# Kernel optimization log

Measured on AMD Instinct MI355X. Metric: run time of the kernel, lower is better.

Reference implementation:

```python
import jax, jax.numpy as jnp
import numpy as np

WEIGHT_SP = 0.1
BANDWIDTH = 0.5
EPS = 1e-5


def _l2_normalize(v, axis, eps=1e-12):
    # matches torch F.normalize(p=2): x / max(||x||, eps)
    n = jnp.sqrt(jnp.sum(v * v, axis=axis, keepdims=True))
    return v / jnp.maximum(n, eps)


def _compute_meshgrid(N, H, W):
    rows = jnp.arange(H, dtype=jnp.float32) / (H + 1)
    cols = jnp.arange(W, dtype=jnp.float32) / (W + 1)
    gr, gc = jnp.meshgrid(rows, cols, indexing="ij")
    grid = jnp.stack([gr, gc])[None]  # (1, 2, H, W)
    return jnp.broadcast_to(grid, (N, 2, H, W))


def _l2_distance(x, y):
    # Faithful to the torch code; its broadcasting is only valid for N == 1.
    N, C, H, W = x.shape
    xv = x.reshape(N, C, -1)
    yv = y.reshape(N, C, -1)
    x_s = jnp.sum(xv ** 2, axis=1)          # (N, HW)
    y_s = jnp.sum(yv ** 2, axis=1)          # (N, HW)
    A = jnp.einsum("nci,ncj->nij", yv, xv)  # (N, HW, HW)
    dist = y_s - 2.0 * A + x_s.T            # same broadcast as torch (N==1)
    dist = jnp.swapaxes(dist, 1, 2)         # transpose(1,2); reshape is no-op
    return jnp.maximum(dist, 0.0)


def _cosine_distance(x, y):
    y_mu = jnp.mean(y, axis=(0, 2, 3), keepdims=True)   # (1, C, 1, 1)
    xn = _l2_normalize(x - y_mu, axis=1)
    yn = _l2_normalize(y - y_mu, axis=1)
    N, C = x.shape[:2]
    xn = xn.reshape(N, C, -1)
    yn = yn.reshape(N, C, -1)
    cos = jnp.einsum("nci,ncj->nij", xn, yn)            # (N, HW, HW)
    return 1.0 - cos


def _relative_distance(dist, eps=1e-5):
    dmin = jnp.min(dist, axis=2, keepdims=True)
    return dist / (dmin + eps)


def _compute_cx(dist_tilde, bandwidth):
    w = jnp.exp((1.0 - dist_tilde) / bandwidth)
    return w / jnp.sum(w, axis=2, keepdims=True)


def setup_inputs() -> dict:
    key = jax.random.key(0)
    k1, k2 = jax.random.split(key)
    x = jax.random.normal(k1, (1, 512, 80, 80), dtype=jnp.float32)
    y = jax.random.normal(k2, (1, 512, 80, 80), dtype=jnp.float32)
    return {"x": x, "y": y}


def reference(x, y):
    N, C, H, W = x.shape
    # spatial branch
    grid = _compute_meshgrid(N, H, W)
    cx_sp = _compute_cx(_relative_distance(_l2_distance(grid, grid), 1e-5), BANDWIDTH)
    # feature branch (loss_type == 'cosine')
    cx_feat = _compute_cx(_relative_distance(_cosine_distance(x, y), EPS), BANDWIDTH)
    cx_combine = (1.0 - WEIGHT_SP) * cx_feat + WEIGHT_SP * cx_sp
    k_max = jnp.max(cx_combine, axis=2, keepdims=True)  # (N, HW, 1)
    cx = jnp.mean(k_max, axis=1)                        # (N, 1)
    return jnp.mean(-jnp.log(cx + EPS))
```

## Files before the change

### kernel.cpp

```cpp
#include <hip/hip_runtime.h>
#include <hip/hip_bf16.h>
#include <math.h>

#define HW 6400
#define NC 512
#define NH 80
#define NW 80
#define NCH 25
#define NSLOT 50
#define NCYS 8
#define JCH 256
#define TI 128
#define BK 64
#define NT16 400

typedef __attribute__((ext_vector_type(8))) short short8;
typedef __attribute__((ext_vector_type(4))) float v4f;

#define MU_OFF    0
#define INVD_OFF  512
#define GMAXP_OFF (512 + HW)
#define ZP_OFF    (GMAXP_OFF + HW*NSLOT)
#define WDP_OFF   (ZP_OFF + HW*NSLOT)
#define ACC_OFF   (WDP_OFF + HW*NCYS)
#define F32_FLOATS (ACC_OFF + 64)
#define XB_BYTE   ((size_t)(((F32_FLOATS*4) + 255) & ~255))
#define YB_BYTE   (XB_BYTE + (size_t)HW*NC*2)
#define G_BYTE    (YB_BYTE + (size_t)HW*NC*2)
#define G_BYTES   ((size_t)NT16 * NT16 * 256 * 2)

typedef __attribute__((address_space(1))) unsigned int uint_g;
typedef __attribute__((address_space(3))) unsigned int uint_l;
__device__ __forceinline__ void gload16(const void* g, void* l) {
    __builtin_amdgcn_global_load_lds((const uint_g*)g, (uint_l*)l, 16, 0, 0);
}

__global__ void k_mu(const float* __restrict__ y, float* __restrict__ mu) {
    int c = blockIdx.x;
    const float* yc = y + (size_t)c * HW;
    float s = 0.f;
    for (int i = threadIdx.x; i < HW; i += 256) s += yc[i];
    __shared__ float red[256];
    red[threadIdx.x] = s;
    __syncthreads();
    for (int off = 128; off > 0; off >>= 1) {
        if (threadIdx.x < off) red[threadIdx.x] += red[threadIdx.x + off];
        __syncthreads();
    }
    if (threadIdx.x == 0) mu[c] = red[0] * (1.0f / HW);
}

__global__ void k_sumsq(const float* __restrict__ x, const float* __restrict__ y,
                        const float* __restrict__ mu,
                        float* __restrict__ psx, float* __restrict__ psy) {
    int i = blockIdx.x * 256 + threadIdx.x;
    int c0 = blockIdx.y * 64;
    float sx = 0.f, sy = 0.f;
    for (int c = c0; c < c0 + 64; ++c) {
        float m = mu[c];
        float dx = x[(size_t)c * HW + i] - m;
        float dy = y[(size_t)c * HW + i] - m;
        sx = fmaf(dx, dx, sx);
        sy = fmaf(dy, dy, sy);
    }
    psx[(size_t)blockIdx.y * HW + i] = sx;
    psy[(size_t)blockIdx.y * HW + i] = sy;
}

__global__ void k_transpose(const float* __restrict__ x, const float* __restrict__ y,
                            const float* __restrict__ mu,
                            const float* __restrict__ psx, const float* __restrict__ psy,
                            unsigned short* __restrict__ xb, unsigned short* __restrict__ yb) {
    __shared__ float tile[64 * 68];
    __shared__ float ssinv[64];
    const int t = threadIdx.x;
    const int i0 = blockIdx.x * 64;
    const int c0 = blockIdx.y * 64;
    const int z = blockIdx.z;
    const float* src = z ? y : x;
    const float* ps  = z ? psy : psx;
    unsigned short* dst = z ? yb : xb;

    if (t < 64) {
        float s = 0.f;
        #pragma unroll
        for (int p = 0; p < 8; ++p) s += ps[(size_t)p * HW + i0 + t];
        ssinv[t] = 1.0f / fmaxf(sqrtf(s), 1e-12f);
    }
    __syncthreads();
    #pragma unroll 4
    for (int it = 0; it < 16; ++it) {
        int cl = it * 4 + (t >> 6);
        int il = t & 63;
        float v = (src[(size_t)(c0 + cl) * HW + i0 + il] - mu[c0 + cl]) * ssinv[il];
        tile[il * 68 + cl] = v;
    }
    __syncthreads();
    #pragma unroll
    for (int it = 0; it < 2; ++it) {
        int il = t >> 2;
        int seg = (t & 3) + it * 4;
        unsigned int pk[4];
        #pragma unroll
        for (int p = 0; p < 4; ++p) {
            float v0 = tile[il * 68 + seg * 8 + p * 2];
            float v1 = tile[il * 68 + seg * 8 + p * 2 + 1];
            __hip_bfloat16 h0 = __float2bfloat16(v0);
            __hip_bfloat16 h1 = __float2bfloat16(v1);
            unsigned short u0 = *reinterpret_cast<unsigned short*>(&h0);
            unsigned short u1 = *reinterpret_cast<unsigned short*>(&h1);
            pk[p] = (unsigned int)u0 | ((unsigned int)u1 << 16);
        }
        uint4 val = make_uint4(pk[0], pk[1], pk[2], pk[3]);
        *(uint4*)&dst[(size_t)(i0 + il) * NC + c0 + seg * 8] = val;
    }
}

template <typename F>
__device__ __forceinline__ void gemm_driver(const unsigned short* __restrict__ Xb,
                                            const unsigned short* __restrict__ Yb,
                                            F&& consume) {
    __shared__ char sA[TI * BK * 2];
    __shared__ char sB[TI * BK * 2];
    const int t = threadIdx.x;
    const int w = t >> 6, l = t & 63;
    const int wr = w >> 1, wc = w & 1;
    const int lr = l & 15, lg = l >> 4;
    const int i0 = blockIdx.x * TI;
    const int jbase = blockIdx.y * JCH;

    int aoff[4][2], boff[4][2];
    #pragma unroll
    for (int mt = 0; mt < 4; ++mt) {
        int row = wr * 64 + mt * 16 + lr;
        #pragma unroll
        for (int ks = 0; ks < 2; ++ks) {
            int seg = ks * 4 + lg;
            aoff[mt][ks] = row * 128 + ((seg ^ (row & 7)) * 16);
        }
    }
    #pragma unroll
    for (int nt = 0; nt < 4; ++nt) {
        int row = wc * 64 + nt * 16 + lr;
        #pragma unroll
        for (int ks = 0; ks < 2; ++ks) {
            int seg = ks * 4 + lg;
            boff[nt][ks] = row * 128 + ((seg ^ (row & 7)) * 16);
        }
    }

    const int strow = l >> 3;
    const int stcol = ((l & 7) ^ strow) * 8;
    char* dA0 = sA + (w * 4 + 0) * 1024;
    char* dA1 = sA + (w * 4 + 1) * 1024;
    char* dA2 = sA + (w * 4 + 2) * 1024;
    char* dA3 = sA + (w * 4 + 3) * 1024;
    char* dB0 = sB + (w * 4 + 0) * 1024;
    char* dB1 = sB + (w * 4 + 1) * 1024;
    char* dB2 = sB + (w * 4 + 2) * 1024;
    char* dB3 = sB + (w * 4 + 3) * 1024;
    const unsigned short* ga = Xb + (size_t)(i0 + w * 32 + strow) * NC + stcol;
    const unsigned short* gb0 = Yb + (size_t)(jbase + w * 32 + strow) * NC + stcol;

    #pragma unroll 1
    for (int jt = 0; jt < JCH; jt += TI) {
        const unsigned short* gb = gb0 + (size_t)jt * NC;
        v4f acc[4][4];
        #pragma unroll
        for (int mt = 0; mt < 4; ++mt)
            #pragma unroll
            for (int nt = 0; nt < 4; ++nt)
                acc[mt][nt] = (v4f){0.f, 0.f, 0.f, 0.f};

        #pragma unroll 1
        for (int kt = 0; kt < NC; kt += BK) {
            __syncthreads();
            gload16(ga + kt,           dA0);
            gload16(ga + 8  * NC + kt, dA1);
            gload16(ga + 16 * NC + kt, dA2);
            gload16(ga + 24 * NC + kt, dA3);
            gload16(gb + kt,           dB0);
            gload16(gb + 8  * NC + kt, dB1);
            gload16(gb + 16 * NC + kt, dB2);
            gload16(gb + 24 * NC + kt, dB3);
            __syncthreads();
            #pragma unroll
            for (int ks = 0; ks < 2; ++ks) {
                short8 af[4], bf[4];
                #pragma unroll
                for (int mt = 0; mt < 4; ++mt) af[mt] = *(const short8*)&sA[aoff[mt][ks]];
                #pragma unroll
                for (int nt = 0; nt < 4; ++nt) bf[nt] = *(const short8*)&sB[boff[nt][ks]];
                #pragma unroll
                for (int mt = 0; mt < 4; ++mt)
                    #pragma unroll
                    for (int nt = 0; nt < 4; ++nt)
                        acc[mt][nt] = __builtin_amdgcn_mfma_f32_16x16x32_bf16(
                            af[mt], bf[nt], acc[mt][nt], 0, 0, 0);
            }
        }
        consume(acc, jt);
    }
}

__device__ __forceinline__ void rmax_epilogue(float (&rmax)[16], float* gmaxp,
                                              int i0, int wr, int wc, int lr, int lg) {
    #pragma unroll
    for (int u = 0; u < 16; ++u) {
        float v = rmax[u];
        v = fmaxf(v, __shfl_xor(v, 1));
        v = fmaxf(v, __shfl_xor(v, 2));
        v = fmaxf(v, __shfl_xor(v, 4));
        v = fmaxf(v, __shfl_xor(v, 8));
        if (lr == 0) {
            int row = i0 + wr * 64 + (u >> 2) * 16 + lg * 4 + (u & 3);
            gmaxp[(size_t)row * NSLOT + blockIdx.y * 2 + wc] = v;
        }
    }
}

__global__ __launch_bounds__(256, 2) void k_pass1s(const unsigned short* __restrict__ Xb,
                                                   const unsigned short* __restrict__ Yb,
                                                   float* __restrict__ gmaxp,
                                                   unsigned int* __restrict__ G2) {
    const int t = threadIdx.x;
    const int w = t >> 6, l = t & 63;
    const int wr = w >> 1, wc = w & 1;
    const int lr = l & 15, lg = l >> 4;
    const int i0 = blockIdx.x * TI;
    const int jbase = blockIdx.y * JCH;
    float rmax[16];
    #pragma unroll
    for (int u = 0; u < 16; ++u) rmax[u] = -3.0e38f;

    gemm_driver(Xb, Yb, [&](v4f (&acc)[4][4], int jt) {
        #pragma unroll
        for (int mt = 0; mt < 4; ++mt) {
            size_t rbase = (size_t)(i0 / 16 + wr * 4 + mt) * (NT16 * 128);
            #pragma unroll
            for (int nt = 0; nt < 4; ++nt) {
                int ct = (jbase + jt) / 16 + wc * 4 + nt;
                unsigned int pk0, pk1;
                {
                    __hip_bfloat16 h0 = __float2bfloat16(acc[mt][nt][0]);
                    __hip_bfloat16 h1 = __float2bfloat16(acc[mt][nt][1]);
                    __hip_bfloat16 h2 = __float2bfloat16(acc[mt][nt][2]);
                    __hip_bfloat16 h3 = __float2bfloat16(acc[mt][nt][3]);
                    pk0 = (unsigned int)*(unsigned short*)&h0 | ((unsigned int)*(unsigned short*)&h1 << 16);
                    pk1 = (unsigned int)*(unsigned short*)&h2 | ((unsigned int)*(unsigned short*)&h3 << 16);
                }
                *(uint2*)&G2[(rbase + (size_t)ct * 128 + l * 2)] = make_uint2(pk0, pk1);
                #pragma unroll
                for (int r = 0; r < 4; ++r)
                    rmax[mt * 4 + r] = fmaxf(rmax[mt * 4 + r], acc[mt][nt][r]);
            }
        }
    });
    rmax_epilogue(rmax, gmaxp, i0, wr, wc, lr, lg);
}

__global__ __launch_bounds__(256) void k_pass2s(const unsigned int* __restrict__ G2,
                                                const float* __restrict__ gmaxp,
                                                float* __restrict__ zp,
                                                float* __restrict__ wdp) {
    const int t = threadIdx.x;
    const int w = t >> 6, l = t & 63;
    const int lr = l & 15, lg = l >> 4;
    const int rt = blockIdx.x * 4 + w;
    const int cy = blockIdx.y;

    float m = -3.0e38f;
    {
        int row = rt * 16 + lr;
        #pragma unroll
        for (int k = 0; k < 13; ++k) {
            int s = lg + 4 * k;
            if (s < NSLOT) m = fmaxf(m, gmaxp[(size_t)row * NSLOT + s]);
        }
        m = fmaxf(m, __shfl_xor(m, 16));
        m = fmaxf(m, __shfl_xor(m, 32));
    }
    float inv_lr = 1.0f / ((1.0f - m) + 1e-5f);
    float c1[4], c2[4];
    #pragma unroll
    for (int r = 0; r < 4; ++r) {
        float iv = __shfl(inv_lr, lg * 4 + r);
        c2[r] = 2.0f * iv;
        c1[r] = 2.0f - 2.0f * iv;
    }

    const uint2* base = (const uint2*)G2 + (size_t)rt * (NT16 * 64) + l;
    float zs[4] = {0.f, 0.f, 0.f, 0.f};
    #pragma unroll 4
    for (int ct = cy * 50; ct < cy * 50 + 50; ++ct) {
        uint2 v = base[(size_t)ct * 64];
        float g0 = __uint_as_float((v.x & 0xFFFFu) << 16);
        float g1 = __uint_as_float(v.x & 0xFFFF0000u);
        float g2 = __uint_as_float((v.y & 0xFFFFu) << 16);
        float g3 = __uint_as_float(v.y & 0xFFFF0000u);
        zs[0] += __expf(fmaf(c2[0], g0, c1[0]));
        zs[1] += __expf(fmaf(c2[1], g1, c1[1]));
        zs[2] += __expf(fmaf(c2[2], g2, c1[2]));
        zs[3] += __expf(fmaf(c2[3], g3, c1[3]));
    }
    float wd[4] = {0.f, 0.f, 0.f, 0.f};
    if (rt / 50 == cy) {
        uint2 v = base[(size_t)rt * 64];
        float g[4];
        g[0] = __uint_as_float((v.x & 0xFFFFu) << 16);
        g[1] = __uint_as_float(v.x & 0xFFFF0000u);
        g[2] = __uint_as_float((v.y & 0xFFFFu) << 16);
        g[3] = __uint_as_float(v.y & 0xFFFF0000u);
        #pragma unroll
        for (int r = 0; r < 4; ++r)
            if (lr == lg * 4 + r) wd[r] = __expf(fmaf(c2[r], g[r], c1[r]));
    }
    #pragma unroll
    for (int r = 0; r < 4; ++r) {
        float z = zs[r], d = wd[r];
        z += __shfl_xor(z, 1);  d += __shfl_xor(d, 1);
        z += __shfl_xor(z, 2);  d += __shfl_xor(d, 2);
        z += __shfl_xor(z, 4);  d += __shfl_xor(d, 4);
        z += __shfl_xor(z, 8);  d += __shfl_xor(d, 8);
        if (lr == 0) {
            int row = rt * 16 + lg * 4 + r;
            zp[(size_t)row * NCYS + cy] = z;
            wdp[(size_t)row * NCYS + cy] = d;
        }
    }
}

__global__ void k_kmax_s(const float* __restrict__ zp, const float* __restrict__ wdp,
                         const float* __restrict__ gmaxp, float* __restrict__ accum,
                         int* __restrict__ counter, float* __restrict__ out) {
    int i = blockIdx.x * 256 + threadIdx.x;
    float Z = 0.f, wd = 0.f, gmax = -3.0e38f;
    #pragma unroll
    for (int s = 0; s < NCYS; ++s) {
        Z += zp[(size_t)i * NCYS + s];
        wd += wdp[(size_t)i * NCYS + s];
    }
    #pragma unroll
    for (int s = 0; s < NSLOT; ++s) gmax = fmaxf(gmax, gmaxp[(size_t)i * NSLOT + s]);
    float dmin = 1.0f - gmax;
    float inv = 1.0f / (dmin + 1e-5f);
    float wmx = __expf(2.0f - 2.0f * dmin * inv);
    float invZ = 1.0f / Z;
    float kmax = fmaxf(0.9f * wmx * invZ, 0.9f * wd * invZ + 0.1f);

    __shared__ float red[256];
    red[threadIdx.x] = kmax;
    __syncthreads();
    for (int off = 128; off > 0; off >>= 1) {
        if (threadIdx.x < off) red[threadIdx.x] += red[threadIdx.x + off];
        __syncthreads();
    }
    if (threadIdx.x == 0) {
        atomicAdd(accum, red[0]);
        __threadfence();
        int n = atomicAdd(counter, 1);
        if (n == (int)gridDim.x - 1) {
            float total = atomicAdd(accum, 0.0f);
            out[0] = -logf(total * (1.0f / HW) + 1e-5f);
        }
    }
}

__global__ __launch_bounds__(256, 2) void k_pass1(const unsigned short* __restrict__ Xb,
                                                  const unsigned short* __restrict__ Yb,
                                                  float* __restrict__ gmaxp) {
    const int t = threadIdx.x;
    const int w = t >> 6, l = t & 63;
    const int wr = w >> 1, wc = w & 1;
    const int lr = l & 15, lg = l >> 4;
    const int i0 = blockIdx.x * TI;
    float rmax[16];
    #pragma unroll
    for (int u = 0; u < 16; ++u) rmax[u] = -3.0e38f;
    gemm_driver(Xb, Yb, [&](v4f (&acc)[4][4], int jt) {
        (void)jt;
        #pragma unroll
        for (int mt = 0; mt < 4; ++mt)
            #pragma unroll
            for (int r = 0; r < 4; ++r) {
                float mm = acc[mt][0][r];
                #pragma unroll
                for (int nt = 1; nt < 4; ++nt) mm = fmaxf(mm, acc[mt][nt][r]);
                rmax[mt * 4 + r] = fmaxf(rmax[mt * 4 + r], mm);
            }
    });
    rmax_epilogue(rmax, gmaxp, i0, wr, wc, lr, lg);
}

__global__ void k_invd(const float* __restrict__ gmaxp, float* __restrict__ invd) {
    int i = blockIdx.x * 256 + threadIdx.x;
    float m = -3.0e38f;
    #pragma unroll
    for (int s = 0; s < NSLOT; ++s) m = fmaxf(m, gmaxp[(size_t)i * NSLOT + s]);
    invd[i] = 1.0f / ((1.0f - m) + 1e-5f);
}

__global__ __launch_bounds__(256, 2) void k_pass2(const unsigned short* __restrict__ Xb,
                                                  const unsigned short* __restrict__ Yb,
                                                  const float* __restrict__ invd,
                                                  float* __restrict__ zp) {
    const int t = threadIdx.x;
    const int w = t >> 6, l = t & 63;
    const int wr = w >> 1, wc = w & 1;
    const int lr = l & 15, lg = l >> 4;
    const int i0 = blockIdx.x * TI;
    float zs[16], c1[16], c2[16];
    #pragma unroll
    for (int u = 0; u < 16; ++u) {
        int row = i0 + wr * 64 + (u >> 2) * 16 + lg * 4 + (u & 3);
        float inv = invd[row];
        c2[u] = 2.0f * inv;
        c1[u] = 2.0f - 2.0f * inv;
        zs[u] = 0.f;
    }
    gemm_driver(Xb, Yb, [&](v4f (&acc)[4][4], int jt) {
        (void)jt;
        #pragma unroll
        for (int mt = 0; mt < 4; ++mt)
            #pragma unroll
            for (int r = 0; r < 4; ++r) {
                int u = mt * 4 + r;
                float s = 0.f;
                #pragma unroll
                for (int nt = 0; nt < 4; ++nt)
                    s += __expf(fmaf(c2[u], acc[mt][nt][r], c1[u]));
                zs[u] += s;
            }
    });
    #pragma unroll
    for (int u = 0; u < 16; ++u) {
        float z = zs[u];
        z += __shfl_xor(z, 1);
        z += __shfl_xor(z, 2);
        z += __shfl_xor(z, 4);
        z += __shfl_xor(z, 8);
        if (lr == 0) {
            int row = i0 + wr * 64 + (u >> 2) * 16 + lg * 4 + (u & 3);
            zp[(size_t)row * NSLOT + blockIdx.y * 2 + wc] = z;
        }
    }
}

__global__ void k_kmax(const float* __restrict__ zp, const float* __restrict__ gmaxp,
                       const unsigned short* __restrict__ Xb, const unsigned short* __restrict__ Yb,
                       float* __restrict__ accum, int* __restrict__ counter,
                       float* __restrict__ out) {
    int i = blockIdx.x * 256 + threadIdx.x;
    float Z = 0.f, gmax = -3.0e38f;
    #pragma unroll
    for (int s = 0; s < NSLOT; ++s) {
        Z += zp[(size_t)i * NSLOT + s];
        gmax = fmaxf(gmax, gmaxp[(size_t)i * NSLOT + s]);
    }
    float gii = 0.f;
    const uint2* xr = (const uint2*)(Xb + (size_t)i * NC);
    const uint2* yr = (const uint2*)(Yb + (size_t)i * NC);
    for (int c4 = 0; c4 < NC / 4; ++c4) {
        uint2 xa = xr[c4], ya = yr[c4];
        float x0 = __uint_as_float((xa.x & 0xFFFFu) << 16), y0 = __uint_as_float((ya.x & 0xFFFFu) << 16);
        float x1 = __uint_as_float(xa.x & 0xFFFF0000u),     y1 = __uint_as_float(ya.x & 0xFFFF0000u);
        float x2 = __uint_as_float((xa.y & 0xFFFFu) << 16), y2 = __uint_as_float((ya.y & 0xFFFFu) << 16);
        float x3 = __uint_as_float(xa.y & 0xFFFF0000u),     y3 = __uint_as_float(ya.y & 0xFFFF0000u);
        gii = fmaf(x0, y0, gii); gii = fmaf(x1, y1, gii);
        gii = fmaf(x2, y2, gii); gii = fmaf(x3, y3, gii);
    }
    float dmin = 1.0f - gmax;
    float inv = 1.0f / (dmin + 1e-5f);
    float wmx = __expf(2.0f - 2.0f * dmin * inv);
    float wii = __expf(2.0f - 2.0f * (1.0f - gii) * inv);
    float invZ = 1.0f / Z;
    float kmax = fmaxf(0.9f * wmx * invZ, 0.9f * wii * invZ + 0.1f);

    __shared__ float red[256];
    red[threadIdx.x] = kmax;
    __syncthreads();
    for (int off = 128; off > 0; off >>= 1) {
        if (threadIdx.x < off) red[threadIdx.x] += red[threadIdx.x + off];
        __syncthreads();
    }
    if (threadIdx.x == 0) {
        atomicAdd(accum, red[0]);
        __threadfence();
        int n = atomicAdd(counter, 1);
        if (n == (int)gridDim.x - 1) {
            float total = atomicAdd(accum, 0.0f);
            out[0] = -logf(total * (1.0f / HW) + 1e-5f);
        }
    }
}

extern "C" void kernel_launch(void* const* d_in, const int* in_sizes, int n_in,
                              void* d_out, int out_size, void* d_ws, size_t ws_size,
                              hipStream_t stream) {
    const float* x = (const float*)d_in[0];
    const float* y = (const float*)d_in[1];
    float* out = (float*)d_out;
    float* ws = (float*)d_ws;

    float* mu    = ws + MU_OFF;
    float* invd  = ws + INVD_OFF;
    float* gmaxp = ws + GMAXP_OFF;
    float* psx   = ws + GMAXP_OFF;
    float* psy   = ws + GMAXP_OFF + 8 * HW;
    float* zp    = ws + ZP_OFF;
    float* wdp   = ws + WDP_OFF;
    float* accum = ws + ACC_OFF;
    int*   counter = (int*)(accum + 1);
    unsigned short* Xb = (unsigned short*)((char*)d_ws + XB_BYTE);
    unsigned short* Yb = (unsigned short*)((char*)d_ws + YB_BYTE);
    unsigned int*   G2 = (unsigned int*)((char*)d_ws + G_BYTE);

    const bool bigws = ws_size >= (G_BYTE + G_BYTES);

    hipMemsetAsync(accum, 0, 8, stream);

    hipLaunchKernelGGL(k_mu, dim3(NC), dim3(256), 0, stream, y, mu);
    hipLaunchKernelGGL(k_sumsq, dim3(HW / 256, NC / 64), dim3(256), 0, stream, x, y, mu, psx, psy);
    hipLaunchKernelGGL(k_transpose, dim3(HW / 64, NC / 64, 2), dim3(256), 0, stream,
                       x, y, mu, psx, psy, Xb, Yb);

    dim3 grid(HW / TI, NCH);
    if (bigws) {
        hipLaunchKernelGGL(k_pass1s, grid, dim3(256), 0, stream, Xb, Yb, gmaxp, G2);
        hipLaunchKernelGGL(k_pass2s, dim3(NT16 / 4, NCYS), dim3(256), 0, stream, G2, gmaxp, zp, wdp);
        hipLaunchKernelGGL(k_kmax_s, dim3(HW / 256), dim3(256), 0, stream, zp, wdp, gmaxp,
                           accum, counter, out);
    } else {
        hipLaunchKernelGGL(k_pass1, grid, dim3(256), 0, stream, Xb, Yb, gmaxp);
        hipLaunchKernelGGL(k_invd, dim3(HW / 256), dim3(256), 0, stream, gmaxp, invd);
        hipLaunchKernelGGL(k_pass2, grid, dim3(256), 0, stream, Xb, Yb, invd, zp);
        hipLaunchKernelGGL(k_kmax, dim3(HW / 256), dim3(256), 0, stream, zp, gmaxp, Xb, Yb,
                           accum, counter, out);
    }
}
```

Baseline: 166.2 us.

## Fuse sum-of-squares into transpose and apply normalization in GEMM epilogue

Removes the separate sum-of-squares kernel: the transpose kernel now accumulates per-pixel squared norms via atomics from its shared tile, and a small kernel converts them to inverse norms. The bf16 operands are stored unnormalized, and the inverse norms are applied to the GEMM outputs in the epilogues. The big-workspace pass1 is rewritten as a standalone kernel with a 128x256 tile that computes the full K loop in one accumulator set, with no inner column loop. This trades one full read of x and y and a launch for atomics, a larger register and LDS footprint, and a different rounding point for the normalization.

```diff
diff --git a/kernel.cpp b/kernel.cpp
--- a/kernel.cpp
+++ b/kernel.cpp
@@ -18,12 +18,14 @@
 typedef __attribute__((ext_vector_type(4))) float v4f;
 
 #define MU_OFF    0
-#define INVD_OFF  512
-#define GMAXP_OFF (512 + HW)
-#define ZP_OFF    (GMAXP_OFF + HW*NSLOT)
+#define SQX_OFF   512
+#define SQY_OFF   (512 + HW)
+#define ACC_OFF   (512 + 2*HW)
+#define GMAXP_OFF (ACC_OFF + 64)
+#define INVD_OFF  (GMAXP_OFF + HW*NSLOT)
+#define ZP_OFF    (INVD_OFF + HW)
 #define WDP_OFF   (ZP_OFF + HW*NSLOT)
-#define ACC_OFF   (WDP_OFF + HW*NCYS)
-#define F32_FLOATS (ACC_OFF + 64)
+#define F32_FLOATS (WDP_OFF + HW*NCYS)
 #define XB_BYTE   ((size_t)(((F32_FLOATS*4) + 255) & ~255))
 #define YB_BYTE   (XB_BYTE + (size_t)HW*NC*2)
 #define G_BYTE    (YB_BYTE + (size_t)HW*NC*2)
@@ -50,52 +52,37 @@
     if (threadIdx.x == 0) mu[c] = red[0] * (1.0f / HW);
 }
 
-__global__ void k_sumsq(const float* __restrict__ x, const float* __restrict__ y,
-                        const float* __restrict__ mu,
-                        float* __restrict__ psx, float* __restrict__ psy) {
-    int i = blockIdx.x * 256 + threadIdx.x;
-    int c0 = blockIdx.y * 64;
-    float sx = 0.f, sy = 0.f;
-    for (int c = c0; c < c0 + 64; ++c) {
-        float m = mu[c];
-        float dx = x[(size_t)c * HW + i] - m;
-        float dy = y[(size_t)c * HW + i] - m;
-        sx = fmaf(dx, dx, sx);
-        sy = fmaf(dy, dy, sy);
-    }
-    psx[(size_t)blockIdx.y * HW + i] = sx;
-    psy[(size_t)blockIdx.y * HW + i] = sy;
-}
-
 __global__ void k_transpose(const float* __restrict__ x, const float* __restrict__ y,
                             const float* __restrict__ mu,
-                            const float* __restrict__ psx, const float* __restrict__ psy,
+                            float* __restrict__ sqx, float* __restrict__ sqy,
                             unsigned short* __restrict__ xb, unsigned short* __restrict__ yb) {
     __shared__ float tile[64 * 68];
-    __shared__ float ssinv[64];
     const int t = threadIdx.x;
     const int i0 = blockIdx.x * 64;
     const int c0 = blockIdx.y * 64;
     const int z = blockIdx.z;
     const float* src = z ? y : x;
-    const float* ps  = z ? psy : psx;
+    float* sq = z ? sqy : sqx;
     unsigned short* dst = z ? yb : xb;
 
-    if (t < 64) {
-        float s = 0.f;
-        #pragma unroll
-        for (int p = 0; p < 8; ++p) s += ps[(size_t)p * HW + i0 + t];
-        ssinv[t] = 1.0f / fmaxf(sqrtf(s), 1e-12f);
-    }
-    __syncthreads();
     #pragma unroll 4
     for (int it = 0; it < 16; ++it) {
         int cl = it * 4 + (t >> 6);
         int il = t & 63;
-        float v = (src[(size_t)(c0 + cl) * HW + i0 + il] - mu[c0 + cl]) * ssinv[il];
+        float v = src[(size_t)(c0 + cl) * HW + i0 + il] - mu[c0 + cl];
         tile[il * 68 + cl] = v;
     }
     __syncthreads();
+    {
+        int il = t & 63, q = t >> 6;
+        float s = 0.f;
+        #pragma unroll
+        for (int cl = q * 16; cl < q * 16 + 16; ++cl) {
+            float v = tile[il * 68 + cl];
+            s = fmaf(v, v, s);
+        }
+        atomicAdd(&sq[i0 + il], s);
+    }
     #pragma unroll
     for (int it = 0; it < 2; ++it) {
         int il = t >> 2;
@@ -113,6 +100,252 @@
         }
         uint4 val = make_uint4(pk[0], pk[1], pk[2], pk[3]);
         *(uint4*)&dst[(size_t)(i0 + il) * NC + c0 + seg * 8] = val;
+    }
+}
+
+__global__ void k_normfin(float* __restrict__ sqx, float* __restrict__ sqy) {
+    int i = blockIdx.x * 256 + threadIdx.x;
+    sqx[i] = 1.0f / fmaxf(sqrtf(sqx[i]), 1e-12f);
+    sqy[i] = 1.0f / fmaxf(sqrtf(sqy[i]), 1e-12f);
+}
+
+__device__ __forceinline__ void rmax_epilogue(float (&rmax)[16], float* gmaxp,
+                                              int i0, int wr, int wc, int lr, int lg) {
+    #pragma unroll
+    for (int u = 0; u < 16; ++u) {
+        float v = rmax[u];
+        v = fmaxf(v, __shfl_xor(v, 1));
+        v = fmaxf(v, __shfl_xor(v, 2));
+        v = fmaxf(v, __shfl_xor(v, 4));
+        v = fmaxf(v, __shfl_xor(v, 8));
+        if (lr == 0) {
+            int row = i0 + wr * 64 + (u >> 2) * 16 + lg * 4 + (u & 3);
+            gmaxp[(size_t)row * NSLOT + blockIdx.y * 2 + wc] = v;
+        }
+    }
+}
+
+__global__ __launch_bounds__(256, 2) void k_pass1s(const unsigned short* __restrict__ Xb,
+                                                   const unsigned short* __restrict__ Yb,
+                                                   const float* __restrict__ sxi,
+                                                   const float* __restrict__ syi,
+                                                   float* __restrict__ gmaxp,
+                                                   unsigned int* __restrict__ G2) {
+    __shared__ char sA[128 * 128];
+    __shared__ char sB[256 * 128];
+    const int t = threadIdx.x;
+    const int w = t >> 6, l = t & 63;
+    const int wr = w >> 1, wc = w & 1;
+    const int lr = l & 15, lg = l >> 4;
+    const int i0 = blockIdx.x * TI;
+    const int jbase = blockIdx.y * JCH;
+
+    int aoff[4][2], boff[8][2];
+    #pragma unroll
+    for (int mt = 0; mt < 4; ++mt) {
+        int row = wr * 64 + mt * 16 + lr;
+        #pragma unroll
+        for (int ks = 0; ks < 2; ++ks) {
+            int seg = ks * 4 + lg;
+            aoff[mt][ks] = row * 128 + ((seg ^ (row & 7)) * 16);
+        }
+    }
+    #pragma unroll
+    for (int nt = 0; nt < 8; ++nt) {
+        int row = wc * 128 + nt * 16 + lr;
+        #pragma unroll
+        for (int ks = 0; ks < 2; ++ks) {
+            int seg = ks * 4 + lg;
+            boff[nt][ks] = row * 128 + ((seg ^ (row & 7)) * 16);
+        }
+    }
+
+    const int strow = l >> 3;
+    const int stcol = ((l & 7) ^ strow) * 8;
+    const unsigned short* ga = Xb + (size_t)(i0 + w * 32 + strow) * NC + stcol;
+    const unsigned short* gb = Yb + (size_t)(jbase + w * 64 + strow) * NC + stcol;
+    char* dA = sA + w * 4096;
+    char* dB = sB + w * 8192;
+
+    v4f acc[4][8];
+    #pragma unroll
+    for (int mt = 0; mt < 4; ++mt)
+        #pragma unroll
+        for (int nt = 0; nt < 8; ++nt)
+            acc[mt][nt] = (v4f){0.f, 0.f, 0.f, 0.f};
+
+    #pragma unroll 1
+    for (int kt = 0; kt < NC; kt += BK) {
+        __syncthreads();
+        gload16(ga + kt,           dA);
+        gload16(ga + 8  * NC + kt, dA + 1024);
+        gload16(ga + 16 * NC + kt, dA + 2048);
+        gload16(ga + 24 * NC + kt, dA + 3072);
+        #pragma unroll
+        for (int it = 0; it < 8; ++it)
+            gload16(gb + it * 8 * NC + kt, dB + it * 1024);
+        __syncthreads();
+        #pragma unroll
+        for (int ks = 0; ks < 2; ++ks) {
+            short8 af[4], bf[8];
+            #pragma unroll
+            for (int mt = 0; mt < 4; ++mt) af[mt] = *(const short8*)&sA[aoff[mt][ks]];
+            #pragma unroll
+            for (int nt = 0; nt < 8; ++nt) bf[nt] = *(const short8*)&sB[boff[nt][ks]];
+            #pragma unroll
+            for (int mt = 0; mt < 4; ++mt)
+                #pragma unroll
+                for (int nt = 0; nt < 8; ++nt)
+                    acc[mt][nt] = __builtin_amdgcn_mfma_f32_16x16x32_bf16(
+                        af[mt], bf[nt], acc[mt][nt], 0, 0, 0);
+        }
+    }
+
+    float rsx[16];
+    #pragma unroll
+    for (int u = 0; u < 16; ++u) {
+        int row = i0 + wr * 64 + (u >> 2) * 16 + lg * 4 + (u & 3);
+        rsx[u] = sxi[row];
+    }
+    float rsy[8];
+    #pragma unroll
+    for (int nt = 0; nt < 8; ++nt)
+        rsy[nt] = syi[jbase + wc * 128 + nt * 16 + lr];
+
+    float rmax[16];
+    #pragma unroll
+    for (int u = 0; u < 16; ++u) rmax[u] = -3.0e38f;
+
+    #pragma unroll
+    for (int mt = 0; mt < 4; ++mt) {
+        size_t rbase = (size_t)(i0 / 16 + wr * 4 + mt) * (NT16 * 128);
+        #pragma unroll
+        for (int nt = 0; nt < 8; ++nt) {
+            int ct = jbase / 16 + wc * 8 + nt;
+            float g0 = acc[mt][nt][0] * rsx[mt * 4 + 0] * rsy[nt];
+            float g1 = acc[mt][nt][1] * rsx[mt * 4 + 1] * rsy[nt];
+            float g2 = acc[mt][nt][2] * rsx[mt * 4 + 2] * rsy[nt];
+            float g3 = acc[mt][nt][3] * rsx[mt * 4 + 3] * rsy[nt];
+            rmax[mt * 4 + 0] = fmaxf(rmax[mt * 4 + 0], g0);
+            rmax[mt * 4 + 1] = fmaxf(rmax[mt * 4 + 1], g1);
+            rmax[mt * 4 + 2] = fmaxf(rmax[mt * 4 + 2], g2);
+            rmax[mt * 4 + 3] = fmaxf(rmax[mt * 4 + 3], g3);
+            __hip_bfloat16 h0 = __float2bfloat16(g0);
+            __hip_bfloat16 h1 = __float2bfloat16(g1);
+            __hip_bfloat16 h2 = __float2bfloat16(g2);
+            __hip_bfloat16 h3 = __float2bfloat16(g3);
+            unsigned int pk0 = (unsigned int)*(unsigned short*)&h0 | ((unsigned int)*(unsigned short*)&h1 << 16);
+            unsigned int pk1 = (unsigned int)*(unsigned short*)&h2 | ((unsigned int)*(unsigned short*)&h3 << 16);
+            *(uint2*)&G2[rbase + (size_t)ct * 128 + l * 2] = make_uint2(pk0, pk1);
+        }
+    }
+    rmax_epilogue(rmax, gmaxp, i0, wr, wc, lr, lg);
+}
+
+__global__ __launch_bounds__(256) void k_pass2s(const unsigned int* __restrict__ G2,
+                                                const float* __restrict__ gmaxp,
+                                                float* __restrict__ zp,
+                                                float* __restrict__ wdp) {
+    const int t = threadIdx.x;
+    const int w = t >> 6, l = t & 63;
+    const int lr = l & 15, lg = l >> 4;
+    const int rt = blockIdx.x * 4 + w;
+    const int cy = blockIdx.y;
+
+    float m = -3.0e38f;
+    {
+        int row = rt * 16 + lr;
+        #pragma unroll
+        for (int k = 0; k < 13; ++k) {
+            int s = lg + 4 * k;
+            if (s < NSLOT) m = fmaxf(m, gmaxp[(size_t)row * NSLOT + s]);
+        }
+        m = fmaxf(m, __shfl_xor(m, 16));
+        m = fmaxf(m, __shfl_xor(m, 32));
+    }
+    float inv_lr = 1.0f / ((1.0f - m) + 1e-5f);
+    float c1[4], c2[4];
+    #pragma unroll
+    for (int r = 0; r < 4; ++r) {
+        float iv = __shfl(inv_lr, lg * 4 + r);
+        c2[r] = 2.0f * iv;
+        c1[r] = 2.0f - 2.0f * iv;
+    }
+
+    const uint2* base = (const uint2*)G2 + (size_t)rt * (NT16 * 64) + l;
+    float zs[4] = {0.f, 0.f, 0.f, 0.f};
+    #pragma unroll 4
+    for (int ct = cy * 50; ct < cy * 50 + 50; ++ct) {
+        uint2 v = base[(size_t)ct * 64];
+        float g0 = __uint_as_float((v.x & 0xFFFFu) << 16);
+        float g1 = __uint_as_float(v.x & 0xFFFF0000u);
+        float g2 = __uint_as_float((v.y & 0xFFFFu) << 16);
+        float g3 = __uint_as_float(v.y & 0xFFFF0000u);
+        zs[0] += __expf(fmaf(c2[0], g0, c1[0]));
+        zs[1] += __expf(fmaf(c2[1], g1, c1[1]));
+        zs[2] += __expf(fmaf(c2[2], g2, c1[2]));
+        zs[3] += __expf(fmaf(c2[3], g3, c1[3]));
+    }
+    float wd[4] = {0.f, 0.f, 0.f, 0.f};
+    if (rt / 50 == cy) {
+        uint2 v = base[(size_t)rt * 64];
+        float g[4];
+        g[0] = __uint_as_float((v.x & 0xFFFFu) << 16);
+        g[1] = __uint_as_float(v.x & 0xFFFF0000u);
+        g[2] = __uint_as_float((v.y & 0xFFFFu) << 16);
+        g[3] = __uint_as_float(v.y & 0xFFFF0000u);
+        #pragma unroll
+        for (int r = 0; r < 4; ++r)
+            if (lr == lg * 4 + r) wd[r] = __expf(fmaf(c2[r], g[r], c1[r]));
+    }
+    #pragma unroll
+    for (int r = 0; r < 4; ++r) {
+        float z = zs[r], d = wd[r];
+        z += __shfl_xor(z, 1);  d += __shfl_xor(d, 1);
+        z += __shfl_xor(z, 2);  d += __shfl_xor(d, 2);
+        z += __shfl_xor(z, 4);  d += __shfl_xor(d, 4);
+        z += __shfl_xor(z, 8);  d += __shfl_xor(d, 8);
+        if (lr == 0) {
+            int row = rt * 16 + lg * 4 + r;
+            zp[(size_t)row * NCYS + cy] = z;
+            wdp[(size_t)row * NCYS + cy] = d;
+        }
+    }
+}
+
+__global__ void k_kmax_s(const float* __restrict__ zp, const float* __restrict__ wdp,
+                         const float* __restrict__ gmaxp, float* __restrict__ accum,
+                         int* __restrict__ counter, float* __restrict__ out) {
+    int i = blockIdx.x * 256 + threadIdx.x;
+    float Z = 0.f, wd = 0.f, gmax = -3.0e38f;
+    #pragma unroll
+    for (int s = 0; s < NCYS; ++s) {
+        Z += zp[(size_t)i * NCYS + s];
+        wd += wdp[(size_t)i * NCYS + s];
+    }
+    #pragma unroll
+    for (int s = 0; s < NSLOT; ++s) gmax = fmaxf(gmax, gmaxp[(size_t)i * NSLOT + s]);
+    float dmin = 1.0f - gmax;
+    float inv = 1.0f / (dmin + 1e-5f);
+    float wmx = __expf(2.0f - 2.0f * dmin * inv);
+    float invZ = 1.0f / Z;
+    float kmax = fmaxf(0.9f * wmx * invZ, 0.9f * wd * invZ + 0.1f);
+
+    __shared__ float red[256];
+    red[threadIdx.x] = kmax;
+    __syncthreads();
+    for (int off = 128; off > 0; off >>= 1) {
+        if (threadIdx.x < off) red[threadIdx.x] += red[threadIdx.x + off];
+        __syncthreads();
+    }
+    if (threadIdx.x == 0) {
+        atomicAdd(accum, red[0]);
+        __threadfence();
+        int n = atomicAdd(counter, 1);
+        if (n == (int)gridDim.x - 1) {
+            float total = atomicAdd(accum, 0.0f);
+            out[0] = -logf(total * (1.0f / HW) + 1e-5f);
+        }
     }
 }
 
@@ -148,7 +381,6 @@
             boff[nt][ks] = row * 128 + ((seg ^ (row & 7)) * 16);
         }
     }
-
     const int strow = l >> 3;
     const int stcol = ((l & 7) ^ strow) * 8;
     char* dA0 = sA + (w * 4 + 0) * 1024;
@@ -203,191 +435,35 @@
     }
 }
 
-__device__ __forceinline__ void rmax_epilogue(float (&rmax)[16], float* gmaxp,
-                                              int i0, int wr, int wc, int lr, int lg) {
-    #pragma unroll
-    for (int u = 0; u < 16; ++u) {
-        float v = rmax[u];
-        v = fmaxf(v, __shfl_xor(v, 1));
-        v = fmaxf(v, __shfl_xor(v, 2));
-        v = fmaxf(v, __shfl_xor(v, 4));
-        v = fmaxf(v, __shfl_xor(v, 8));
-        if (lr == 0) {
-            int row = i0 + wr * 64 + (u >> 2) * 16 + lg * 4 + (u & 3);
-            gmaxp[(size_t)row * NSLOT + blockIdx.y * 2 + wc] = v;
-        }
-    }
-}
-
-__global__ __launch_bounds__(256, 2) void k_pass1s(const unsigned short* __restrict__ Xb,
-                                                   const unsigned short* __restrict__ Yb,
-                                                   float* __restrict__ gmaxp,
-                                                   unsigned int* __restrict__ G2) {
+__global__ __launch_bounds__(256, 2) void k_pass1(const unsigned short* __restrict__ Xb,
+                                                  const unsigned short* __restrict__ Yb,
+                                                  const float* __restrict__ sxi,
+                                                  const float* __restrict__ syi,
+                                                  float* __restrict__ gmaxp) {
     const int t = threadIdx.x;
     const int w = t >> 6, l = t & 63;
     const int wr = w >> 1, wc = w & 1;
     const int lr = l & 15, lg = l >> 4;
     const int i0 = blockIdx.x * TI;
     const int jbase = blockIdx.y * JCH;
-    float rmax[16];
-    #pragma unroll
-    for (int u = 0; u < 16; ++u) rmax[u] = -3.0e38f;
-
+    float rsx[16], rmax[16];
+    #pragma unroll
+    for (int u = 0; u < 16; ++u) {
+        int row = i0 + wr * 64 + (u >> 2) * 16 + lg * 4 + (u & 3);
+        rsx[u] = sxi[row];
+        rmax[u] = -3.0e38f;
+    }
     gemm_driver(Xb, Yb, [&](v4f (&acc)[4][4], int jt) {
         #pragma unroll
-        for (int mt = 0; mt < 4; ++mt) {
-            size_t rbase = (size_t)(i0 / 16 + wr * 4 + mt) * (NT16 * 128);
+        for (int nt = 0; nt < 4; ++nt) {
+            float sy = syi[jbase + jt + (wc * 4 + nt) * 16 + lr];
             #pragma unroll
-            for (int nt = 0; nt < 4; ++nt) {
-                int ct = (jbase + jt) / 16 + wc * 4 + nt;
-                unsigned int pk0, pk1;
-                {
-                    __hip_bfloat16 h0 = __float2bfloat16(acc[mt][nt][0]);
-                    __hip_bfloat16 h1 = __float2bfloat16(acc[mt][nt][1]);
-                    __hip_bfloat16 h2 = __float2bfloat16(acc[mt][nt][2]);
-                    __hip_bfloat16 h3 = __float2bfloat16(acc[mt][nt][3]);
-                    pk0 = (unsigned int)*(unsigned short*)&h0 | ((unsigned int)*(unsigned short*)&h1 << 16);
-                    pk1 = (unsigned int)*(unsigned short*)&h2 | ((unsigned int)*(unsigned short*)&h3 << 16);
-                }
-                *(uint2*)&G2[(rbase + (size_t)ct * 128 + l * 2)] = make_uint2(pk0, pk1);
+            for (int mt = 0; mt < 4; ++mt)
                 #pragma unroll
                 for (int r = 0; r < 4; ++r)
-                    rmax[mt * 4 + r] = fmaxf(rmax[mt * 4 + r], acc[mt][nt][r]);
-            }
-        }
-    });
-    rmax_epilogue(rmax, gmaxp, i0, wr, wc, lr, lg);
-}
-
-__global__ __launch_bounds__(256) void k_pass2s(const unsigned int* __restrict__ G2,
-                                                const float* __restrict__ gmaxp,
-                                                float* __restrict__ zp,
-                                                float* __restrict__ wdp) {
-    const int t = threadIdx.x;
-    const int w = t >> 6, l = t & 63;
-    const int lr = l & 15, lg = l >> 4;
-    const int rt = blockIdx.x * 4 + w;
-    const int cy = blockIdx.y;
-
-    float m = -3.0e38f;
-    {
-        int row = rt * 16 + lr;
-        #pragma unroll
-        for (int k = 0; k < 13; ++k) {
-            int s = lg + 4 * k;
-            if (s < NSLOT) m = fmaxf(m, gmaxp[(size_t)row * NSLOT + s]);
-        }
-        m = fmaxf(m, __shfl_xor(m, 16));
-        m = fmaxf(m, __shfl_xor(m, 32));
-    }
-    float inv_lr = 1.0f / ((1.0f - m) + 1e-5f);
-    float c1[4], c2[4];
-    #pragma unroll
-    for (int r = 0; r < 4; ++r) {
-        float iv = __shfl(inv_lr, lg * 4 + r);
-        c2[r] = 2.0f * iv;
-        c1[r] = 2.0f - 2.0f * iv;
-    }
-
-    const uint2* base = (const uint2*)G2 + (size_t)rt * (NT16 * 64) + l;
-    float zs[4] = {0.f, 0.f, 0.f, 0.f};
-    #pragma unroll 4
-    for (int ct = cy * 50; ct < cy * 50 + 50; ++ct) {
-        uint2 v = base[(size_t)ct * 64];
-        float g0 = __uint_as_float((v.x & 0xFFFFu) << 16);
-        float g1 = __uint_as_float(v.x & 0xFFFF0000u);
-        float g2 = __uint_as_float((v.y & 0xFFFFu) << 16);
-        float g3 = __uint_as_float(v.y & 0xFFFF0000u);
-        zs[0] += __expf(fmaf(c2[0], g0, c1[0]));
-        zs[1] += __expf(fmaf(c2[1], g1, c1[1]));
-        zs[2] += __expf(fmaf(c2[2], g2, c1[2]));
-        zs[3] += __expf(fmaf(c2[3], g3, c1[3]));
-    }
-    float wd[4] = {0.f, 0.f, 0.f, 0.f};
-    if (rt / 50 == cy) {
-        uint2 v = base[(size_t)rt * 64];
-        float g[4];
-        g[0] = __uint_as_float((v.x & 0xFFFFu) << 16);
-        g[1] = __uint_as_float(v.x & 0xFFFF0000u);
-        g[2] = __uint_as_float((v.y & 0xFFFFu) << 16);
-        g[3] = __uint_as_float(v.y & 0xFFFF0000u);
-        #pragma unroll
-        for (int r = 0; r < 4; ++r)
-            if (lr == lg * 4 + r) wd[r] = __expf(fmaf(c2[r], g[r], c1[r]));
-    }
-    #pragma unroll
-    for (int r = 0; r < 4; ++r) {
-        float z = zs[r], d = wd[r];
-        z += __shfl_xor(z, 1);  d += __shfl_xor(d, 1);
-        z += __shfl_xor(z, 2);  d += __shfl_xor(d, 2);
-        z += __shfl_xor(z, 4);  d += __shfl_xor(d, 4);
-        z += __shfl_xor(z, 8);  d += __shfl_xor(d, 8);
-        if (lr == 0) {
-            int row = rt * 16 + lg * 4 + r;
-            zp[(size_t)row * NCYS + cy] = z;
-            wdp[(size_t)row * NCYS + cy] = d;
-        }
-    }
-}
-
-__global__ void k_kmax_s(const float* __restrict__ zp, const float* __restrict__ wdp,
-                         const float* __restrict__ gmaxp, float* __restrict__ accum,
-                         int* __restrict__ counter, float* __restrict__ out) {
-    int i = blockIdx.x * 256 + threadIdx.x;
-    float Z = 0.f, wd = 0.f, gmax = -3.0e38f;
-    #pragma unroll
-    for (int s = 0; s < NCYS; ++s) {
-        Z += zp[(size_t)i * NCYS + s];
-        wd += wdp[(size_t)i * NCYS + s];
-    }
-    #pragma unroll
-    for (int s = 0; s < NSLOT; ++s) gmax = fmaxf(gmax, gmaxp[(size_t)i * NSLOT + s]);
-    float dmin = 1.0f - gmax;
-    float inv = 1.0f / (dmin + 1e-5f);
-    float wmx = __expf(2.0f - 2.0f * dmin * inv);
-    float invZ = 1.0f / Z;
-    float kmax = fmaxf(0.9f * wmx * invZ, 0.9f * wd * invZ + 0.1f);
-
-    __shared__ float red[256];
-    red[threadIdx.x] = kmax;
-    __syncthreads();
-    for (int off = 128; off > 0; off >>= 1) {
-        if (threadIdx.x < off) red[threadIdx.x] += red[threadIdx.x + off];
-        __syncthreads();
-    }
-    if (threadIdx.x == 0) {
-        atomicAdd(accum, red[0]);
-        __threadfence();
-        int n = atomicAdd(counter, 1);
-        if (n == (int)gridDim.x - 1) {
-            float total = atomicAdd(accum, 0.0f);
-            out[0] = -logf(total * (1.0f / HW) + 1e-5f);
-        }
-    }
-}
-
-__global__ __launch_bounds__(256, 2) void k_pass1(const unsigned short* __restrict__ Xb,
-                                                  const unsigned short* __restrict__ Yb,
-                                                  float* __restrict__ gmaxp) {
-    const int t = threadIdx.x;
-    const int w = t >> 6, l = t & 63;
-    const int wr = w >> 1, wc = w & 1;
-    const int lr = l & 15, lg = l >> 4;
-    const int i0 = blockIdx.x * TI;
-    float rmax[16];
-    #pragma unroll
-    for (int u = 0; u < 16; ++u) rmax[u] = -3.0e38f;
-    gemm_driver(Xb, Yb, [&](v4f (&acc)[4][4], int jt) {
-        (void)jt;
-        #pragma unroll
-        for (int mt = 0; mt < 4; ++mt)
-            #pragma unroll
-            for (int r = 0; r < 4; ++r) {
-                float mm = acc[mt][0][r];
-                #pragma unroll
-                for (int nt = 1; nt < 4; ++nt) mm = fmaxf(mm, acc[mt][nt][r]);
-                rmax[mt * 4 + r] = fmaxf(rmax[mt * 4 + r], mm);
-            }
+                    rmax[mt * 4 + r] = fmaxf(rmax[mt * 4 + r],
+                                             acc[mt][nt][r] * rsx[mt * 4 + r] * sy);
+        }
     });
     rmax_epilogue(rmax, gmaxp, i0, wr, wc, lr, lg);
 }
@@ -402,6 +478,8 @@
 
 __global__ __launch_bounds__(256, 2) void k_pass2(const unsigned short* __restrict__ Xb,
                                                   const unsigned short* __restrict__ Yb,
+                                                  const float* __restrict__ sxi,
+                                                  const float* __restrict__ syi,
                                                   const float* __restrict__ invd,
                                                   float* __restrict__ zp) {
     const int t = threadIdx.x;
@@ -409,28 +487,30 @@
     const int wr = w >> 1, wc = w & 1;
     const int lr = l & 15, lg = l >> 4;
     const int i0 = blockIdx.x * TI;
-    float zs[16], c1[16], c2[16];
+    const int jbase = blockIdx.y * JCH;
+    float zs[16], c1[16], c2[16], rsx[16];
     #pragma unroll
     for (int u = 0; u < 16; ++u) {
         int row = i0 + wr * 64 + (u >> 2) * 16 + lg * 4 + (u & 3);
         float inv = invd[row];
         c2[u] = 2.0f * inv;
         c1[u] = 2.0f - 2.0f * inv;
+        rsx[u] = sxi[row];
         zs[u] = 0.f;
     }
     gemm_driver(Xb, Yb, [&](v4f (&acc)[4][4], int jt) {
-        (void)jt;
-        #pragma unroll
-        for (int mt = 0; mt < 4; ++mt)
+        #pragma unroll
+        for (int nt = 0; nt < 4; ++nt) {
+            float sy = syi[jbase + jt + (wc * 4 + nt) * 16 + lr];
             #pragma unroll
-            for (int r = 0; r < 4; ++r) {
-                int u = mt * 4 + r;
-                float s = 0.f;
+            for (int mt = 0; mt < 4; ++mt)
                 #pragma unroll
-                for (int nt = 0; nt < 4; ++nt)
-                    s += __expf(fmaf(c2[u], acc[mt][nt][r], c1[u]));
-                zs[u] += s;
-            }
+                for (int r = 0; r < 4; ++r) {
+                    int u = mt * 4 + r;
+                    float g = acc[mt][nt][r] * rsx[u] * sy;
+                    zs[u] += __expf(fmaf(c2[u], g, c1[u]));
+                }
+        }
     });
     #pragma unroll
     for (int u = 0; u < 16; ++u) {
@@ -448,6 +528,7 @@
 
 __global__ void k_kmax(const float* __restrict__ zp, const float* __restrict__ gmaxp,
                        const unsigned short* __restrict__ Xb, const unsigned short* __restrict__ Yb,
+                       const float* __restrict__ sxi, const float* __restrict__ syi,
                        float* __restrict__ accum, int* __restrict__ counter,
                        float* __restrict__ out) {
     int i = blockIdx.x * 256 + threadIdx.x;
@@ -469,6 +550,7 @@
         gii = fmaf(x0, y0, gii); gii = fmaf(x1, y1, gii);
         gii = fmaf(x2, y2, gii); gii = fmaf(x3, y3, gii);
     }
+    gii *= sxi[i] * syi[i];
     float dmin = 1.0f - gmax;
     float inv = 1.0f / (dmin + 1e-5f);
     float wmx = __expf(2.0f - 2.0f * dmin * inv);
@@ -503,38 +585,38 @@
     float* ws = (float*)d_ws;
 
     float* mu    = ws + MU_OFF;
+    float* sqx   = ws + SQX_OFF;
+    float* sqy   = ws + SQY_OFF;
+    float* accum = ws + ACC_OFF;
+    int*   counter = (int*)(accum + 1);
+    float* gmaxp = ws + GMAXP_OFF;
     float* invd  = ws + INVD_OFF;
-    float* gmaxp = ws + GMAXP_OFF;
-    float* psx   = ws + GMAXP_OFF;
-    float* psy   = ws + GMAXP_OFF + 8 * HW;
     float* zp    = ws + ZP_OFF;
     float* wdp   = ws + WDP_OFF;
-    float* accum = ws + ACC_OFF;
-    int*   counter = (int*)(accum + 1);
     unsigned short* Xb = (unsigned short*)((char*)d_ws + XB_BYTE);
     unsigned short* Yb = (unsigned short*)((char*)d_ws + YB_BYTE);
     unsigned int*   G2 = (unsigned int*)((char*)d_ws + G_BYTE);
 
     const bool bigws = ws_size >= (G_BYTE + G_BYTES);
 
-    hipMemsetAsync(accum, 0, 8, stream);
+    hipMemsetAsync(sqx, 0, (2 * HW + 64) * sizeof(float), stream);
 
     hipLaunchKernelGGL(k_mu, dim3(NC), dim3(256), 0, stream, y, mu);
-    hipLaunchKernelGGL(k_sumsq, dim3(HW / 256, NC / 64), dim3(256), 0, stream, x, y, mu, psx, psy);
     hipLaunchKernelGGL(k_transpose, dim3(HW / 64, NC / 64, 2), dim3(256), 0, stream,
-                       x, y, mu, psx, psy, Xb, Yb);
+                       x, y, mu, sqx, sqy, Xb, Yb);
+    hipLaunchKernelGGL(k_normfin, dim3(HW / 256), dim3(256), 0, stream, sqx, sqy);
 
     dim3 grid(HW / TI, NCH);
     if (bigws) {
-        hipLaunchKernelGGL(k_pass1s, grid, dim3(256), 0, stream, Xb, Yb, gmaxp, G2);
+        hipLaunchKernelGGL(k_pass1s, grid, dim3(256), 0, stream, Xb, Yb, sqx, sqy, gmaxp, G2);
         hipLaunchKernelGGL(k_pass2s, dim3(NT16 / 4, NCYS), dim3(256), 0, stream, G2, gmaxp, zp, wdp);
         hipLaunchKernelGGL(k_kmax_s, dim3(HW / 256), dim3(256), 0, stream, zp, wdp, gmaxp,
                            accum, counter, out);
     } else {
-        hipLaunchKernelGGL(k_pass1, grid, dim3(256), 0, stream, Xb, Yb, gmaxp);
+        hipLaunchKernelGGL(k_pass1, grid, dim3(256), 0, stream, Xb, Yb, sqx, sqy, gmaxp);
         hipLaunchKernelGGL(k_invd, dim3(HW / 256), dim3(256), 0, stream, gmaxp, invd);
-        hipLaunchKernelGGL(k_pass2, grid, dim3(256), 0, stream, Xb, Yb, invd, zp);
+        hipLaunchKernelGGL(k_pass2, grid, dim3(256), 0, stream, Xb, Yb, sqx, sqy, invd, zp);
         hipLaunchKernelGGL(k_kmax, dim3(HW / 256), dim3(256), 0, stream, zp, gmaxp, Xb, Yb,
-                           accum, counter, out);
-    }
-}
+                           sqx, sqy, accum, counter, out);
+    }
+}
```

After: 164.1 us. Within noise of the previous version (-1.2%).
